# Optimization experiments

Hardware: AMD Instinct MI355X
Metric: run time of the kernel (lower is better)

The kernel has to match this reference:

```python
import jax, jax.numpy as jnp
import numpy as np

B, T, H, L = 256, 1024, 64, 5  # batch, seq_len, hidden_size, num_layers


def setup_inputs() -> dict:
    key = jax.random.key(0)
    ks = jax.random.split(key, 10)
    s = 1.0 / np.sqrt(H)  # PyTorch LSTM/Linear uniform init bound

    def u(k, shape):
        return jax.random.uniform(k, shape, jnp.float32, -s, s)

    return {
        "x": jax.random.normal(ks[0], (B, T, 1), jnp.float32),
        "w_ih0": u(ks[1], (4 * H, 1)),          # layer 0 input weights (input_size=1)
        "w_ih_rest": u(ks[2], (L - 1, 4 * H, H)),  # layers 1..4 input weights
        "w_hh": u(ks[3], (L, 4 * H, H)),
        "b_ih": u(ks[4], (L, 4 * H)),
        "b_hh": u(ks[5], (L, 4 * H)),
        "W1": u(ks[6], (H, H)),
        "b1": u(ks[7], (H,)),
        "W2": u(ks[8], (1, H)),
        "b2": u(ks[9], (1,)),
        "future": 0,
    }


def _lstm_layer(x, w_ih, w_hh, b_ih, b_hh):
    # x: [B, T, in]; PyTorch gate order i, f, g, o
    gx = jnp.einsum('bti,gi->btg', x, w_ih) + b_ih  # precompute input projections [B,T,4H]
    h0 = jnp.zeros((x.shape[0], w_hh.shape[1]), x.dtype)

    def step(carry, gxt):
        h, c = carry
        gates = gxt + h @ w_hh.T + b_hh  # [B,4H]
        i, f, g, o = jnp.split(gates, 4, axis=-1)
        c = jax.nn.sigmoid(f) * c + jax.nn.sigmoid(i) * jnp.tanh(g)
        h = jax.nn.sigmoid(o) * jnp.tanh(c)
        return (h, c), h

    _, hs = jax.lax.scan(step, (h0, h0), jnp.swapaxes(gx, 0, 1))  # scan over time
    return jnp.swapaxes(hs, 0, 1)  # [B,T,H]


def _model(x, w_ih0, w_ih_rest, w_hh, b_ih, b_hh, W1, b1, W2, b2):
    # 5-layer LSTM (inter-layer dropout=0.1 is inactive in eval mode)
    h = _lstm_layer(x, w_ih0, w_hh[0], b_ih[0], b_hh[0])
    for l in range(1, w_hh.shape[0]):
        h = _lstm_layer(h, w_ih_rest[l - 1], w_hh[l], b_ih[l], b_hh[l])
    h = jax.nn.relu(h)
    h = jax.nn.relu(h @ W1.T + b1)
    return h @ W2.T + b2  # [B,T,1]


def reference(x, w_ih0, w_ih_rest, w_hh, b_ih, b_hh, W1, b1, W2, b2, future):
    out = None
    for _ in range(future + 1):
        out = _model(x, w_ih0, w_ih_rest, w_hh, b_ih, b_hh, W1, b1, W2, b2)
        x = jnp.concatenate([x, out[:, -1:, :]], axis=1)
    return out
```

## Files before the change

kernel.cpp:

```cpp
#include <hip/hip_runtime.h>

#define B_ 256
#define T_ 1024
#define H_ 64

typedef float f32x2 __attribute__((ext_vector_type(2)));
typedef float f32x4 __attribute__((ext_vector_type(4)));

__device__ __forceinline__ float fast_sigmoid(float x) {
    float e = __builtin_amdgcn_exp2f(-1.4426950408889634f * x);
    return __builtin_amdgcn_rcpf(1.0f + e);
}
__device__ __forceinline__ float fast_tanh(float x) {
    float e = __builtin_amdgcn_exp2f(2.8853900817779268f * x);
    return 1.0f - 2.0f * __builtin_amdgcn_rcpf(1.0f + e);
}

template<int CTRL>
__device__ __forceinline__ float dpp_addf(float v) {
    int vi = __builtin_bit_cast(int, v);
    int sh = __builtin_amdgcn_update_dpp(0, vi, CTRL, 0xF, 0xF, true);
    return v + __builtin_bit_cast(float, sh);
}

__device__ __forceinline__ void block_sync_lds() {
    asm volatile("s_waitcnt lgkmcnt(0)\n\ts_barrier" ::: "memory");
}

__device__ __forceinline__ float hsum4(f32x4 v) { return (v.x + v.y) + (v.z + v.w); }

__device__ __forceinline__ void load_w_heavy(const float* __restrict__ w_ih,
                                             const float* __restrict__ w_hh,
                                             int j, int kc, f32x4 wt[4][8]) {
    #pragma unroll
    for (int r = 0; r < 4; ++r) {
        const int row = r * H_ + j;
        const float* base = (kc < 2) ? (w_ih + row * H_ + kc * 32)
                                     : (w_hh + row * H_ + (kc - 2) * 32);
        #pragma unroll
        for (int q = 0; q < 8; ++q)
            wt[r][q] = *(const f32x4*)(base + 4 * q);
    }
    #pragma unroll
    for (int r = 0; r < 4; ++r)
        #pragma unroll
        for (int q = 0; q < 8; ++q)
            asm volatile("" : "+v"(wt[r][q]));
}

__device__ __forceinline__ void dot4x32(const float* chunk, const f32x4 wt[4][8],
                                        float acc[4]) {
    const f32x4* xv = (const f32x4*)chunk;
    f32x4 a0 = {0,0,0,0}, a1 = {0,0,0,0}, a2 = {0,0,0,0}, a3 = {0,0,0,0};
    #pragma unroll
    for (int q = 0; q < 8; ++q) {
        f32x4 hq = xv[q];
        a0 = __builtin_elementwise_fma(wt[0][q], hq, a0);
        a1 = __builtin_elementwise_fma(wt[1][q], hq, a1);
        a2 = __builtin_elementwise_fma(wt[2][q], hq, a2);
        a3 = __builtin_elementwise_fma(wt[3][q], hq, a3);
    }
    acc[0] = hsum4(a0); acc[1] = hsum4(a1);
    acc[2] = hsum4(a2); acc[3] = hsum4(a3);
}

__global__ __attribute__((amdgpu_flat_work_group_size(768, 768)))
void lstm_tri012(const float* __restrict__ x,
                 float* __restrict__ hout,
                 const float* __restrict__ w_ih0,
                 const float* __restrict__ whh0,
                 const float* __restrict__ bih0, const float* __restrict__ bhh0,
                 const float* __restrict__ wih1, const float* __restrict__ whh1,
                 const float* __restrict__ bih1, const float* __restrict__ bhh1,
                 const float* __restrict__ wih2, const float* __restrict__ whh2,
                 const float* __restrict__ bih2, const float* __restrict__ bhh2)
{
    const int b    = blockIdx.x;
    const int tid  = threadIdx.x;
    const int role = tid >> 8;
    const int loc  = tid & 255;
    const int kc   = loc & 3;
    const int j    = loc >> 2;

    __shared__ __align__(16) float bufL0[2][80];
    __shared__ __align__(16) float bufL1[2][144];
    __shared__ __align__(16) float bufL2[2][144];

    f32x4 wt[4][8];
    float bias0 = 0.f, bias1 = 0.f, bias2 = 0.f, bias3 = 0.f;
    float w00 = 0.f, w01 = 0.f, w02 = 0.f, w03 = 0.f;

    if (role == 0) {
        #pragma unroll
        for (int r = 0; r < 4; ++r) {
            const int row = r * H_ + j;
            const float* base = whh0 + row * H_ + kc * 16;
            #pragma unroll
            for (int q = 0; q < 4; ++q)
                wt[r][q] = *(const f32x4*)(base + 4 * q);
        }
        #pragma unroll
        for (int r = 0; r < 4; ++r)
            #pragma unroll
            for (int q = 0; q < 4; ++q)
                asm volatile("" : "+v"(wt[r][q]));
        if (kc == 0) {
            bias0 = bih0[0*H_+j] + bhh0[0*H_+j];
            bias1 = bih0[1*H_+j] + bhh0[1*H_+j];
            bias2 = bih0[2*H_+j] + bhh0[2*H_+j];
            bias3 = bih0[3*H_+j] + bhh0[3*H_+j];
            w00 = w_ih0[0*H_+j]; w01 = w_ih0[1*H_+j];
            w02 = w_ih0[2*H_+j]; w03 = w_ih0[3*H_+j];
        }
    } else {
        const float* wih = (role == 1) ? wih1 : wih2;
        const float* whh = (role == 1) ? whh1 : whh2;
        const float* bih = (role == 1) ? bih1 : bih2;
        const float* bhh = (role == 1) ? bhh1 : bhh2;
        load_w_heavy(wih, whh, j, kc, wt);
        if (kc == 0) {
            bias0 = bih[0*H_+j] + bhh[0*H_+j];
            bias1 = bih[1*H_+j] + bhh[1*H_+j];
            bias2 = bih[2*H_+j] + bhh[2*H_+j];
            bias3 = bih[3*H_+j] + bhh[3*H_+j];
        }
    }
    float c_st = 0.f;
    float xt = (role == 0) ? x[(long)b * T_] : 0.f;

    float (*myBuf)[144] = (role == 1) ? bufL1 : bufL2;

    if (loc < H_) {
        const int u = loc;
        if (role == 0)      bufL0[0][(u >> 4) * 20 + (u & 15)] = 0.f;
        else if (role == 1) bufL1[1][(2 + (u >> 5)) * 36 + (u & 31)] = 0.f;
        else                bufL2[0][(2 + (u >> 5)) * 36 + (u & 31)] = 0.f;
    }
    block_sync_lds();

    for (int s = 0; s <= T_ + 1; ++s) {
        const int rb = s & 1, wb = rb ^ 1;
        const bool active = (role == 0) ? (s < T_)
                          : (role == 1) ? (s >= 1 && s <= T_)
                                        : (s >= 2);
        if (active) {
            if (role == 0) {
                float xn = 0.f;
                if (s + 1 < T_) xn = x[(long)b * T_ + s + 1];
                const f32x4* xv = (const f32x4*)&bufL0[rb][kc * 20];
                f32x4 h0 = xv[0], h1 = xv[1], h2 = xv[2], h3 = xv[3];
                f32x4 a0 = {0,0,0,0}, a1 = {0,0,0,0}, a2 = {0,0,0,0}, a3 = {0,0,0,0};
                a0 = __builtin_elementwise_fma(wt[0][0], h0, a0);
                a1 = __builtin_elementwise_fma(wt[1][0], h0, a1);
                a2 = __builtin_elementwise_fma(wt[2][0], h0, a2);
                a3 = __builtin_elementwise_fma(wt[3][0], h0, a3);
                a0 = __builtin_elementwise_fma(wt[0][1], h1, a0);
                a1 = __builtin_elementwise_fma(wt[1][1], h1, a1);
                a2 = __builtin_elementwise_fma(wt[2][1], h1, a2);
                a3 = __builtin_elementwise_fma(wt[3][1], h1, a3);
                a0 = __builtin_elementwise_fma(wt[0][2], h2, a0);
                a1 = __builtin_elementwise_fma(wt[1][2], h2, a1);
                a2 = __builtin_elementwise_fma(wt[2][2], h2, a2);
                a3 = __builtin_elementwise_fma(wt[3][2], h2, a3);
                a0 = __builtin_elementwise_fma(wt[0][3], h3, a0);
                a1 = __builtin_elementwise_fma(wt[1][3], h3, a1);
                a2 = __builtin_elementwise_fma(wt[2][3], h3, a2);
                a3 = __builtin_elementwise_fma(wt[3][3], h3, a3);
                float acc0 = hsum4(a0), acc1 = hsum4(a1);
                float acc2 = hsum4(a2), acc3 = hsum4(a3);
                acc0 = dpp_addf<0xB1>(acc0); acc1 = dpp_addf<0xB1>(acc1);
                acc2 = dpp_addf<0xB1>(acc2); acc3 = dpp_addf<0xB1>(acc3);
                acc0 = dpp_addf<0x4E>(acc0); acc1 = dpp_addf<0x4E>(acc1);
                acc2 = dpp_addf<0x4E>(acc2); acc3 = dpp_addf<0x4E>(acc3);
                if (kc == 0) {
                    float i_ = fast_sigmoid(acc0 + bias0 + w00 * xt);
                    float f_ = fast_sigmoid(acc1 + bias1 + w01 * xt);
                    float g_ = fast_tanh   (acc2 + bias2 + w02 * xt);
                    float o_ = fast_sigmoid(acc3 + bias3 + w03 * xt);
                    c_st = f_ * c_st + i_ * g_;
                    float h = o_ * fast_tanh(c_st);
                    bufL0[wb][(j >> 4) * 20 + (j & 15)] = h;
                    bufL1[wb][(j >> 5) * 36 + (j & 31)] = h;
                }
                xt = xn;
            } else {
                float acc[4];
                dot4x32(&myBuf[rb][kc * 36], wt, acc);
                acc[0] = dpp_addf<0xB1>(acc[0]); acc[1] = dpp_addf<0xB1>(acc[1]);
                acc[2] = dpp_addf<0xB1>(acc[2]); acc[3] = dpp_addf<0xB1>(acc[3]);
                acc[0] = dpp_addf<0x4E>(acc[0]); acc[1] = dpp_addf<0x4E>(acc[1]);
                acc[2] = dpp_addf<0x4E>(acc[2]); acc[3] = dpp_addf<0x4E>(acc[3]);
                if (kc == 0) {
                    float i_ = fast_sigmoid(acc[0] + bias0);
                    float f_ = fast_sigmoid(acc[1] + bias1);
                    float g_ = fast_tanh   (acc[2] + bias2);
                    float o_ = fast_sigmoid(acc[3] + bias3);
                    c_st = f_ * c_st + i_ * g_;
                    float h = o_ * fast_tanh(c_st);
                    myBuf[wb][(2 + (j >> 5)) * 36 + (j & 31)] = h;
                    if (role == 1)
                        bufL2[wb][(j >> 5) * 36 + (j & 31)] = h;
                    else
                        hout[((long)b * T_ + (s - 2)) * H_ + j] = h;
                }
            }
        }
        block_sync_lds();
    }
}

__global__ __attribute__((amdgpu_flat_work_group_size(512, 512)))
void lstm_pair34(const float* __restrict__ xin,
                 float* __restrict__ hout,
                 const float* __restrict__ wih3, const float* __restrict__ whh3,
                 const float* __restrict__ bih3, const float* __restrict__ bhh3,
                 const float* __restrict__ wih4, const float* __restrict__ whh4,
                 const float* __restrict__ bih4, const float* __restrict__ bhh4)
{
    const int b    = blockIdx.x;
    const int tid  = threadIdx.x;
    const int role = tid >> 8;
    const int loc  = tid & 255;
    const int kc   = loc & 3;
    const int j    = loc >> 2;

    __shared__ __align__(16) float bufL3[2][144];
    __shared__ __align__(16) float bufL4[2][144];

    const float* wih = (role == 0) ? wih3 : wih4;
    const float* whh = (role == 0) ? whh3 : whh4;
    const float* bih = (role == 0) ? bih3 : bih4;
    const float* bhh = (role == 0) ? bhh3 : bhh4;
    float (*myBuf)[144] = (role == 0) ? bufL3 : bufL4;

    f32x4 wt[4][8];
    load_w_heavy(wih, whh, j, kc, wt);

    float bias0 = 0.f, bias1 = 0.f, bias2 = 0.f, bias3 = 0.f;
    if (kc == 0) {
        bias0 = bih[0*H_+j] + bhh[0*H_+j];
        bias1 = bih[1*H_+j] + bhh[1*H_+j];
        bias2 = bih[2*H_+j] + bhh[2*H_+j];
        bias3 = bih[3*H_+j] + bhh[3*H_+j];
    }
    float c_st = 0.f;

    if (tid < H_) {
        const int u = tid;
        bufL3[0][(u >> 5) * 36 + (u & 31)] = xin[(long)b * T_ * H_ + u];
        bufL3[0][(2 + (u >> 5)) * 36 + (u & 31)] = 0.f;
    } else if (tid < 128) {
        const int u = tid - 64;
        bufL4[1][(2 + (u >> 5)) * 36 + (u & 31)] = 0.f;
    }
    block_sync_lds();

    for (int s = 0; s <= T_; ++s) {
        const int rb = s & 1, wb = rb ^ 1;
        const bool active = (role == 0) ? (s < T_) : (s >= 1);
        if (active) {
            float xn = 0.f;
            if (role == 0 && kc == 1 && s + 1 < T_)
                xn = xin[((long)b * T_ + s + 1) * H_ + j];

            float acc[4];
            dot4x32(&myBuf[rb][kc * 36], wt, acc);
            acc[0] = dpp_addf<0xB1>(acc[0]); acc[1] = dpp_addf<0xB1>(acc[1]);
            acc[2] = dpp_addf<0xB1>(acc[2]); acc[3] = dpp_addf<0xB1>(acc[3]);
            acc[0] = dpp_addf<0x4E>(acc[0]); acc[1] = dpp_addf<0x4E>(acc[1]);
            acc[2] = dpp_addf<0x4E>(acc[2]); acc[3] = dpp_addf<0x4E>(acc[3]);

            if (kc == 0) {
                float i_ = fast_sigmoid(acc[0] + bias0);
                float f_ = fast_sigmoid(acc[1] + bias1);
                float g_ = fast_tanh   (acc[2] + bias2);
                float o_ = fast_sigmoid(acc[3] + bias3);
                c_st = f_ * c_st + i_ * g_;
                float h = o_ * fast_tanh(c_st);
                myBuf[wb][(2 + (j >> 5)) * 36 + (j & 31)] = h;
                if (role == 0)
                    bufL4[wb][(j >> 5) * 36 + (j & 31)] = h;
                else
                    hout[((long)b * T_ + (s - 1)) * H_ + j] = h;
            }
            if (role == 0 && kc == 1)
                bufL3[wb][(j >> 5) * 36 + (j & 31)] = xn;
        }
        block_sync_lds();
    }
}

__global__ __launch_bounds__(256)
void mlp_head_v2(const float* __restrict__ hbuf,
                 const float* __restrict__ W1,
                 const float* __restrict__ b1,
                 const float* __restrict__ W2,
                 const float* __restrict__ b2,
                 float* __restrict__ out)
{
    const long r = (long)blockIdx.x * 256 + threadIdx.x;

    float row[H_];
    const float4* src = (const float4*)(hbuf + r * H_);
    #pragma unroll
    for (int q = 0; q < 16; ++q) {
        float4 v = src[q];
        row[4*q+0] = fmaxf(v.x, 0.f); row[4*q+1] = fmaxf(v.y, 0.f);
        row[4*q+2] = fmaxf(v.z, 0.f); row[4*q+3] = fmaxf(v.w, 0.f);
    }
    #pragma unroll
    for (int q = 0; q < 16; ++q)
        asm volatile("" : "+v"(row[4*q]), "+v"(row[4*q+1]),
                         "+v"(row[4*q+2]), "+v"(row[4*q+3]));

    float acc = b2[0];
    for (int jj = 0; jj < H_; ++jj) {
        const float* wrow = W1 + jj * H_;
        float s0 = 0.f, s1 = 0.f, s2 = 0.f, s3 = 0.f;
        #pragma unroll
        for (int q = 0; q < 16; ++q) {
            s0 += row[4*q+0] * wrow[4*q+0];
            s1 += row[4*q+1] * wrow[4*q+1];
            s2 += row[4*q+2] * wrow[4*q+2];
            s3 += row[4*q+3] * wrow[4*q+3];
        }
        float y = fmaxf(b1[jj] + (s0 + s1) + (s2 + s3), 0.f);
        acc += y * W2[jj];
    }
    out[r] = acc;
}

extern "C" void kernel_launch(void* const* d_in, const int* in_sizes, int n_in,
                              void* d_out, int out_size, void* d_ws, size_t ws_size,
                              hipStream_t stream) {
    const float* x     = (const float*)d_in[0];
    const float* w_ih0 = (const float*)d_in[1];
    const float* w_ihr = (const float*)d_in[2];
    const float* w_hh  = (const float*)d_in[3];
    const float* b_ih  = (const float*)d_in[4];
    const float* b_hh  = (const float*)d_in[5];
    const float* W1    = (const float*)d_in[6];
    const float* b1    = (const float*)d_in[7];
    const float* W2    = (const float*)d_in[8];
    const float* b2    = (const float*)d_in[9];

    float* out = (float*)d_out;
    float* buf = (float*)d_ws;

    const long LW = 4L * H_ * H_;
    const long LB = 4L * H_;

    lstm_tri012<<<dim3(B_), dim3(768), 0, stream>>>(
        x, buf,
        w_ih0, w_hh + 0 * LW, b_ih + 0 * LB, b_hh + 0 * LB,
        w_ihr + 0 * LW, w_hh + 1 * LW, b_ih + 1 * LB, b_hh + 1 * LB,
        w_ihr + 1 * LW, w_hh + 2 * LW, b_ih + 2 * LB, b_hh + 2 * LB);

    lstm_pair34<<<dim3(B_), dim3(512), 0, stream>>>(
        buf, buf,
        w_ihr + 2 * LW, w_hh + 3 * LW, b_ih + 3 * LB, b_hh + 3 * LB,
        w_ihr + 3 * LW, w_hh + 4 * LW, b_ih + 4 * LB, b_hh + 4 * LB);

    mlp_head_v2<<<dim3((B_ * T_) / 256), dim3(256), 0, stream>>>(
        buf, W1, b1, W2, b2, out);
}
```

Baseline: 1.713 ms.

## Fuse MLP head into layers 3-4 LSTM kernel as a third pipeline stage

Adds a third wavefront group of 64 threads to the layer 3/4 kernel. It consumes each layer-4 hidden state from shared memory one step later and computes the ReLU-Linear-ReLU-Linear head in place, using DPP and readlane reductions. This removes the separate head kernel and the write and re-read of the full layer-4 hidden sequence in global memory. In exchange the recurrent loop gets one extra step and a larger block, and the head work now runs serially per timestep alongside the recurrence.

```diff
diff --git a/kernel.cpp b/kernel.cpp
--- a/kernel.cpp
+++ b/kernel.cpp
@@ -41,11 +41,6 @@
         for (int q = 0; q < 8; ++q)
             wt[r][q] = *(const f32x4*)(base + 4 * q);
     }
-    #pragma unroll
-    for (int r = 0; r < 4; ++r)
-        #pragma unroll
-        for (int q = 0; q < 8; ++q)
-            asm volatile("" : "+v"(wt[r][q]));
 }
 
 __device__ __forceinline__ void dot4x32(const float* chunk, const f32x4 wt[4][8],
@@ -118,6 +113,11 @@
         const float* bih = (role == 1) ? bih1 : bih2;
         const float* bhh = (role == 1) ? bhh1 : bhh2;
         load_w_heavy(wih, whh, j, kc, wt);
+        #pragma unroll
+        for (int r = 0; r < 4; ++r)
+            #pragma unroll
+            for (int q = 0; q < 8; ++q)
+                asm volatile("" : "+v"(wt[r][q]));
         if (kc == 0) {
             bias0 = bih[0*H_+j] + bhh[0*H_+j];
             bias1 = bih[1*H_+j] + bhh[1*H_+j];
@@ -209,13 +209,17 @@
     }
 }
 
-__global__ __attribute__((amdgpu_flat_work_group_size(512, 512)))
-void lstm_pair34(const float* __restrict__ xin,
-                 float* __restrict__ hout,
-                 const float* __restrict__ wih3, const float* __restrict__ whh3,
-                 const float* __restrict__ bih3, const float* __restrict__ bhh3,
-                 const float* __restrict__ wih4, const float* __restrict__ whh4,
-                 const float* __restrict__ bih4, const float* __restrict__ bhh4)
+__global__ __attribute__((amdgpu_flat_work_group_size(576, 576)))
+void lstm_pair34_head(const float* __restrict__ xin,
+                      float* __restrict__ out,
+                      const float* __restrict__ wih3, const float* __restrict__ whh3,
+                      const float* __restrict__ bih3, const float* __restrict__ bhh3,
+                      const float* __restrict__ wih4, const float* __restrict__ whh4,
+                      const float* __restrict__ bih4, const float* __restrict__ bhh4,
+                      const float* __restrict__ W1,
+                      const float* __restrict__ b1,
+                      const float* __restrict__ W2,
+                      const float* __restrict__ b2)
 {
     const int b    = blockIdx.x;
     const int tid  = threadIdx.x;
@@ -226,24 +230,46 @@
 
     __shared__ __align__(16) float bufL3[2][144];
     __shared__ __align__(16) float bufL4[2][144];
-
-    const float* wih = (role == 0) ? wih3 : wih4;
-    const float* whh = (role == 0) ? whh3 : whh4;
-    const float* bih = (role == 0) ? bih3 : bih4;
-    const float* bhh = (role == 0) ? bhh3 : bhh4;
+    __shared__ __align__(16) float headBuf[2][64];
+
+    f32x4 wt[4][8];
+    float bias0 = 0.f, bias1 = 0.f, bias2 = 0.f, bias3 = 0.f;
+    float b1j = 0.f, w2j = 0.f, b2v = 0.f;
+
+    if (role < 2) {
+        const float* wih = (role == 0) ? wih3 : wih4;
+        const float* whh = (role == 0) ? whh3 : whh4;
+        const float* bih = (role == 0) ? bih3 : bih4;
+        const float* bhh = (role == 0) ? bhh3 : bhh4;
+        load_w_heavy(wih, whh, j, kc, wt);
+        if (kc == 0) {
+            bias0 = bih[0*H_+j] + bhh[0*H_+j];
+            bias1 = bih[1*H_+j] + bhh[1*H_+j];
+            bias2 = bih[2*H_+j] + bhh[2*H_+j];
+            bias3 = bih[3*H_+j] + bhh[3*H_+j];
+        }
+    } else {
+        const int hj = loc & 63;
+        #pragma unroll
+        for (int q = 0; q < 8; ++q) {
+            wt[0][q] = *(const f32x4*)(W1 + hj * H_ + 4 * q);
+            wt[1][q] = *(const f32x4*)(W1 + hj * H_ + 32 + 4 * q);
+            wt[2][q] = (f32x4){0.f, 0.f, 0.f, 0.f};
+            wt[3][q] = (f32x4){0.f, 0.f, 0.f, 0.f};
+        }
+        b1j = b1[hj];
+        w2j = W2[hj];
+        b2v = b2[0];
+    }
+    #pragma unroll
+    for (int r = 0; r < 4; ++r)
+        #pragma unroll
+        for (int q = 0; q < 8; ++q)
+            asm volatile("" : "+v"(wt[r][q]));
+
+    float c_st = 0.f;
+
     float (*myBuf)[144] = (role == 0) ? bufL3 : bufL4;
-
-    f32x4 wt[4][8];
-    load_w_heavy(wih, whh, j, kc, wt);
-
-    float bias0 = 0.f, bias1 = 0.f, bias2 = 0.f, bias3 = 0.f;
-    if (kc == 0) {
-        bias0 = bih[0*H_+j] + bhh[0*H_+j];
-        bias1 = bih[1*H_+j] + bhh[1*H_+j];
-        bias2 = bih[2*H_+j] + bhh[2*H_+j];
-        bias3 = bih[3*H_+j] + bhh[3*H_+j];
-    }
-    float c_st = 0.f;
 
     if (tid < H_) {
         const int u = tid;
@@ -255,79 +281,73 @@
     }
     block_sync_lds();
 
-    for (int s = 0; s <= T_; ++s) {
+    for (int s = 0; s <= T_ + 1; ++s) {
         const int rb = s & 1, wb = rb ^ 1;
-        const bool active = (role == 0) ? (s < T_) : (s >= 1);
-        if (active) {
-            float xn = 0.f;
-            if (role == 0 && kc == 1 && s + 1 < T_)
-                xn = xin[((long)b * T_ + s + 1) * H_ + j];
-
-            float acc[4];
-            dot4x32(&myBuf[rb][kc * 36], wt, acc);
-            acc[0] = dpp_addf<0xB1>(acc[0]); acc[1] = dpp_addf<0xB1>(acc[1]);
-            acc[2] = dpp_addf<0xB1>(acc[2]); acc[3] = dpp_addf<0xB1>(acc[3]);
-            acc[0] = dpp_addf<0x4E>(acc[0]); acc[1] = dpp_addf<0x4E>(acc[1]);
-            acc[2] = dpp_addf<0x4E>(acc[2]); acc[3] = dpp_addf<0x4E>(acc[3]);
-
-            if (kc == 0) {
-                float i_ = fast_sigmoid(acc[0] + bias0);
-                float f_ = fast_sigmoid(acc[1] + bias1);
-                float g_ = fast_tanh   (acc[2] + bias2);
-                float o_ = fast_sigmoid(acc[3] + bias3);
-                c_st = f_ * c_st + i_ * g_;
-                float h = o_ * fast_tanh(c_st);
-                myBuf[wb][(2 + (j >> 5)) * 36 + (j & 31)] = h;
-                if (role == 0)
-                    bufL4[wb][(j >> 5) * 36 + (j & 31)] = h;
-                else
-                    hout[((long)b * T_ + (s - 1)) * H_ + j] = h;
+
+        if (role < 2) {
+            const bool active = (role == 0) ? (s < T_) : (s >= 1 && s <= T_);
+            if (active) {
+                float xn = 0.f;
+                if (role == 0 && kc == 1 && s + 1 < T_)
+                    xn = xin[((long)b * T_ + s + 1) * H_ + j];
+
+                float acc[4];
+                dot4x32(&myBuf[rb][kc * 36], wt, acc);
+                acc[0] = dpp_addf<0xB1>(acc[0]); acc[1] = dpp_addf<0xB1>(acc[1]);
+                acc[2] = dpp_addf<0xB1>(acc[2]); acc[3] = dpp_addf<0xB1>(acc[3]);
+                acc[0] = dpp_addf<0x4E>(acc[0]); acc[1] = dpp_addf<0x4E>(acc[1]);
+                acc[2] = dpp_addf<0x4E>(acc[2]); acc[3] = dpp_addf<0x4E>(acc[3]);
+
+                if (kc == 0) {
+                    float i_ = fast_sigmoid(acc[0] + bias0);
+                    float f_ = fast_sigmoid(acc[1] + bias1);
+                    float g_ = fast_tanh   (acc[2] + bias2);
+                    float o_ = fast_sigmoid(acc[3] + bias3);
+                    c_st = f_ * c_st + i_ * g_;
+                    float h = o_ * fast_tanh(c_st);
+                    myBuf[wb][(2 + (j >> 5)) * 36 + (j & 31)] = h;
+                    if (role == 0)
+                        bufL4[wb][(j >> 5) * 36 + (j & 31)] = h;
+                    else
+                        headBuf[wb][j] = h;
+                }
+                if (role == 0 && kc == 1)
+                    bufL3[wb][(j >> 5) * 36 + (j & 31)] = xn;
             }
-            if (role == 0 && kc == 1)
-                bufL3[wb][(j >> 5) * 36 + (j & 31)] = xn;
+        } else {
+            if (s >= 2) {
+                const int hj = loc & 63;
+                const f32x4* hv = (const f32x4*)&headBuf[rb][0];
+                const f32x4 z4 = {0.f, 0.f, 0.f, 0.f};
+                f32x4 a = z4;
+                #pragma unroll
+                for (int q = 0; q < 8; ++q) {
+                    f32x4 h4 = __builtin_elementwise_max(hv[q], z4);
+                    a = __builtin_elementwise_fma(wt[0][q], h4, a);
+                }
+                #pragma unroll
+                for (int q = 0; q < 8; ++q) {
+                    f32x4 h4 = __builtin_elementwise_max(hv[8 + q], z4);
+                    a = __builtin_elementwise_fma(wt[1][q], h4, a);
+                }
+                float y = fmaxf(b1j + hsum4(a), 0.f);
+                float part = y * w2j;
+                part = dpp_addf<0xB1>(part);
+                part = dpp_addf<0x4E>(part);
+                part = dpp_addf<0x141>(part);
+                part = dpp_addf<0x140>(part);
+                int pi = __builtin_bit_cast(int, part);
+                float tsum =
+                    __builtin_bit_cast(float, __builtin_amdgcn_readlane(pi, 0)) +
+                    __builtin_bit_cast(float, __builtin_amdgcn_readlane(pi, 16)) +
+                    __builtin_bit_cast(float, __builtin_amdgcn_readlane(pi, 32)) +
+                    __builtin_bit_cast(float, __builtin_amdgcn_readlane(pi, 48));
+                if (hj == 0)
+                    out[(long)b * T_ + (s - 2)] = tsum + b2v;
+            }
         }
         block_sync_lds();
     }
-}
-
-__global__ __launch_bounds__(256)
-void mlp_head_v2(const float* __restrict__ hbuf,
-                 const float* __restrict__ W1,
-                 const float* __restrict__ b1,
-                 const float* __restrict__ W2,
-                 const float* __restrict__ b2,
-                 float* __restrict__ out)
-{
-    const long r = (long)blockIdx.x * 256 + threadIdx.x;
-
-    float row[H_];
-    const float4* src = (const float4*)(hbuf + r * H_);
-    #pragma unroll
-    for (int q = 0; q < 16; ++q) {
-        float4 v = src[q];
-        row[4*q+0] = fmaxf(v.x, 0.f); row[4*q+1] = fmaxf(v.y, 0.f);
-        row[4*q+2] = fmaxf(v.z, 0.f); row[4*q+3] = fmaxf(v.w, 0.f);
-    }
-    #pragma unroll
-    for (int q = 0; q < 16; ++q)
-        asm volatile("" : "+v"(row[4*q]), "+v"(row[4*q+1]),
-                         "+v"(row[4*q+2]), "+v"(row[4*q+3]));
-
-    float acc = b2[0];
-    for (int jj = 0; jj < H_; ++jj) {
-        const float* wrow = W1 + jj * H_;
-        float s0 = 0.f, s1 = 0.f, s2 = 0.f, s3 = 0.f;
-        #pragma unroll
-        for (int q = 0; q < 16; ++q) {
-            s0 += row[4*q+0] * wrow[4*q+0];
-            s1 += row[4*q+1] * wrow[4*q+1];
-            s2 += row[4*q+2] * wrow[4*q+2];
-            s3 += row[4*q+3] * wrow[4*q+3];
-        }
-        float y = fmaxf(b1[jj] + (s0 + s1) + (s2 + s3), 0.f);
-        acc += y * W2[jj];
-    }
-    out[r] = acc;
 }
 
 extern "C" void kernel_launch(void* const* d_in, const int* in_sizes, int n_in,
@@ -356,11 +376,9 @@
         w_ihr + 0 * LW, w_hh + 1 * LW, b_ih + 1 * LB, b_hh + 1 * LB,
         w_ihr + 1 * LW, w_hh + 2 * LW, b_ih + 2 * LB, b_hh + 2 * LB);
 
-    lstm_pair34<<<dim3(B_), dim3(512), 0, stream>>>(
-        buf, buf,
+    lstm_pair34_head<<<dim3(B_), dim3(576), 0, stream>>>(
+        buf, out,
         w_ihr + 2 * LW, w_hh + 3 * LW, b_ih + 3 * LB, b_hh + 3 * LB,
-        w_ihr + 3 * LW, w_hh + 4 * LW, b_ih + 4 * LB, b_hh + 4 * LB);
-
-    mlp_head_v2<<<dim3((B_ * T_) / 256), dim3(256), 0, stream>>>(
-        buf, W1, b1, W2, b2, out);
-}
+        w_ihr + 3 * LW, w_hh + 4 * LW, b_ih + 4 * LB, b_hh + 4 * LB,
+        W1, b1, W2, b2);
+}
```

After: 2.035 ms. 18.8% more time.
